# Kernel tuning notes

Hardware: AMD Instinct MI355X
Metric: run time of the kernel (lower is better)

## Reference

```python
import jax, jax.numpy as jnp
import numpy as np
import math

B = 2048
NOSC = 64            # oscillators per modality
M = 3                # modalities (audio, text, vision) in sorted order
BDIM = 256           # binding_dim
DT = 0.01
NSTEPS = 10
DIMS = [512, 768, 1024]  # audio, text, vision
TWO_PI = 2.0 * math.pi


def setup_inputs() -> dict:
    key = jax.random.key(0)
    ks = iter(jax.random.split(key, 40))
    d = {}
    names = ['a', 't', 'v']
    for name, dim, x_key in zip(names, DIMS, ['x_audio', 'x_text', 'x_vision']):
        d[x_key] = jax.random.normal(next(ks), (B, dim), dtype=jnp.float32)
        s = 1.0 / math.sqrt(dim)
        d[f'Wf_{name}'] = jax.random.uniform(next(ks), (BDIM, dim), jnp.float32, -s, s)
        d[f'bf_{name}'] = jax.random.uniform(next(ks), (BDIM,), jnp.float32, -s, s)
        d[f'Wp_{name}'] = jax.random.uniform(next(ks), (NOSC, dim), jnp.float32, -s, s)
        d[f'bp_{name}'] = jax.random.uniform(next(ks), (NOSC,), jnp.float32, -s, s)
    # omegas: randn*0.1 + 1.0 + i*0.5 for i-th sorted modality
    for i, name in enumerate(names):
        d[f'omega_{name}'] = jax.random.normal(next(ks), (NOSC,), jnp.float32) * 0.1 + 1.0 + i * 0.5
    N = M * NOSC
    d['inter_coupling'] = jax.random.normal(next(ks), (N, N), jnp.float32) * 0.1
    s = 1.0 / math.sqrt(BDIM * M)
    d['W_fusion'] = jax.random.uniform(next(ks), (BDIM, BDIM * M), jnp.float32, -s, s)
    d['b_fusion'] = jax.random.uniform(next(ks), (BDIM,), jnp.float32, -s, s)
    return d


def reference(x_audio, x_text, x_vision,
              Wf_a, bf_a, Wp_a, bp_a,
              Wf_t, bf_t, Wp_t, bp_t,
              Wf_v, bf_v, Wp_v, bp_v,
              omega_a, omega_t, omega_v,
              inter_coupling, W_fusion, b_fusion):
    def enc(x, Wf, bf, Wp, bp):
        encoded = x @ Wf.T + bf                       # (B, BDIM)
        phases = (x @ Wp.T + bp) % TWO_PI             # (B, NOSC)
        return encoded, phases

    e_a, p_a = enc(x_audio, Wf_a, bf_a, Wp_a, bp_a)
    e_t, p_t = enc(x_text, Wf_t, bf_t, Wp_t, bp_t)
    e_v, p_v = enc(x_vision, Wf_v, bf_v, Wp_v, bp_v)

    phases = jnp.concatenate([p_a, p_t, p_v], axis=-1)        # (B, N)
    omega = jnp.concatenate([omega_a, omega_t, omega_v])      # (N,)
    K = (inter_coupling + inter_coupling.T) * 0.5             # (N, N)
    N = phases.shape[-1]

    def step(ph, _):
        diff = ph[:, :, None] - ph[:, None, :]                # (B, N, N)
        forces = jnp.einsum('ij,bij->bi', K, jnp.sin(diff)) / N
        ph = (ph + DT * (omega[None, :] + forces)) % TWO_PI
        return ph, None

    phases, _ = jax.lax.scan(step, phases, None, length=NSTEPS)

    pm = [phases[:, i * NOSC:(i + 1) * NOSC] for i in range(M)]  # per-modality

    # PLV between banks a,b: |mean_{i,j} exp(i(a_i - b_j))| = R_a * R_b where
    # R = |mean_k exp(i phi_k)| (resultant length), computed with real math.
    R = jnp.stack([jnp.sqrt(jnp.mean(jnp.cos(p), -1) ** 2 +
                            jnp.mean(jnp.sin(p), -1) ** 2) for p in pm])  # (M, B)
    bm = jnp.mean(R[:, None, :] * R[None, :, :], axis=-1)      # (M, M)
    binding_matrix = jnp.where(jnp.eye(M, dtype=bool), 1.0, bm)

    fused_parts = []
    for e, p in zip([e_a, e_t, e_v], pm):
        phase_mod = jnp.mean(jnp.cos(p), axis=-1, keepdims=True)  # (B, 1)
        fused_parts.append(e * (0.5 + 0.5 * phase_mod))
    fused = jnp.concatenate(fused_parts, axis=-1)              # (B, M*BDIM)
    bound = fused @ W_fusion.T + b_fusion                      # (B, BDIM)

    triu = jnp.triu(jnp.ones((M, M), dtype=bool), k=1)
    total = jnp.sum(jnp.where(triu, binding_matrix, 0.0)) / triu.sum()
    total_binding = jnp.full((bound.shape[0],), total)

    return bound, binding_matrix, phases, total_binding
```

## Files before the change

### kernel.cpp

```cpp
#include <hip/hip_runtime.h>
#include <math.h>

typedef short bf16x8 __attribute__((ext_vector_type(8)));
typedef short bf16x4 __attribute__((ext_vector_type(4)));
typedef float f32x4  __attribute__((ext_vector_type(4)));

#define INV_2PI  0.15915494309189535f
#define TWO_PI_F 6.283185307179586f
#define FSCALE   8.2893199e-06f

static __device__ inline short f2bf(float f) {
    union { float f; unsigned u; } v; v.f = f;
    unsigned r = (v.u + 0x7FFFu + ((v.u >> 16) & 1u)) >> 16;
    return (short)r;
}
static __device__ inline float bf2f(short h) {
    union { unsigned u; float f; } v; v.u = ((unsigned)(unsigned short)h) << 16;
    return v.f;
}

__global__ __launch_bounds__(256) void front_kernel(
    const float* __restrict__ xa, const float* __restrict__ xt, const float* __restrict__ xv,
    const float* __restrict__ Wpa, const float* __restrict__ Wpt, const float* __restrict__ Wpv,
    const float* __restrict__ Wfa, const float* __restrict__ Wft, const float* __restrict__ Wfv,
    const float* __restrict__ Wfu,
    const float* __restrict__ IC,
    const float* __restrict__ oa, const float* __restrict__ ot, const float* __restrict__ ov,
    const float* __restrict__ bpa, const float* __restrict__ bpt, const float* __restrict__ bpv,
    float* __restrict__ partial, short* __restrict__ XB, short* __restrict__ WB,
    short* __restrict__ Kp,
    float* __restrict__ om_eff, float* __restrict__ bp_all, float* __restrict__ bacc)
{
    __shared__ alignas(16) float As[16][72];
    __shared__ alignas(16) float Bs[16][72];
    int b = blockIdx.x;
    int t = threadIdx.x;

    if (b < 576) {
        int slot = b % 18, rb = b / 18;
        int z = slot < 4 ? 0 : (slot < 10 ? 1 : 2);
        int chunk = slot - (z == 0 ? 0 : (z == 1 ? 4 : 10));
        const float* A = z == 0 ? xa : (z == 1 ? xt : xv);
        const float* W = z == 0 ? Wpa : (z == 1 ? Wpt : Wpv);
        short* XBz = XB + (z == 0 ? 0 : (z == 1 ? 1048576 : 2621440));
        int K = z == 0 ? 512 : (z == 1 ? 768 : 1024);
        int kb = chunk * 128;
        int m0 = rb * 64;

        int tx = t & 15, ty = t >> 4;
        int row = t >> 2, c4 = t & 3;

        float acc[4][4] = {};
        float4 ar = *(const float4*)&A[(size_t)(m0 + row) * K + kb + c4 * 4];
        float4 br = *(const float4*)&W[(size_t)row * K + kb + c4 * 4];

        for (int k0 = 0; k0 < 128; k0 += 16) {
            if (k0) __syncthreads();
            As[c4 * 4 + 0][row] = ar.x;
            As[c4 * 4 + 1][row] = ar.y;
            As[c4 * 4 + 2][row] = ar.z;
            As[c4 * 4 + 3][row] = ar.w;
            Bs[c4 * 4 + 0][row] = br.x;
            Bs[c4 * 4 + 1][row] = br.y;
            Bs[c4 * 4 + 2][row] = br.z;
            Bs[c4 * 4 + 3][row] = br.w;
            {
                bf16x4 h; h[0] = f2bf(ar.x); h[1] = f2bf(ar.y);
                h[2] = f2bf(ar.z); h[3] = f2bf(ar.w);
                *(bf16x4*)&XBz[(size_t)(m0 + row) * K + kb + k0 + c4 * 4] = h;
            }
            __syncthreads();
            if (k0 + 16 < 128) {
                ar = *(const float4*)&A[(size_t)(m0 + row) * K + kb + k0 + 16 + c4 * 4];
                br = *(const float4*)&W[(size_t)row * K + kb + k0 + 16 + c4 * 4];
            }
#pragma unroll
            for (int kk = 0; kk < 16; ++kk) {
                float4 aq = *(const float4*)&As[kk][ty * 4];
                float4 bq = *(const float4*)&Bs[kk][tx * 4];
                float av[4] = {aq.x, aq.y, aq.z, aq.w};
                float bv[4] = {bq.x, bq.y, bq.z, bq.w};
#pragma unroll
                for (int i = 0; i < 4; ++i)
#pragma unroll
                    for (int j = 0; j < 4; ++j)
                        acc[i][j] += av[i] * bv[j];
            }
        }

        float* P = partial + (size_t)slot * 131072;
#pragma unroll
        for (int i = 0; i < 4; ++i) {
            float4 v = make_float4(acc[i][0], acc[i][1], acc[i][2], acc[i][3]);
            *(float4*)&P[(size_t)(m0 + ty * 4 + i) * 64 + tx * 4] = v;
        }
    } else if (b < 600) {
        for (int u = (b - 576) * 256 + t; u < 196608; u += 24 * 256) {
            const float4* sp;
            if (u < 32768)       sp = (const float4*)Wfa + u;
            else if (u < 81920)  sp = (const float4*)Wft + (u - 32768);
            else if (u < 147456) sp = (const float4*)Wfv + (u - 81920);
            else                 sp = (const float4*)Wfu + (u - 147456);
            float4 v = *sp;
            bf16x4 h; h[0] = f2bf(v.x); h[1] = f2bf(v.y); h[2] = f2bf(v.z); h[3] = f2bf(v.w);
            *(bf16x4*)(WB + (size_t)u * 4) = h;
        }
    } else if (b < 632) {
        for (int idx = (b - 600) * 256 + t; idx < 36864; idx += 32 * 256) {
            int k = idx / 192, n = idx - k * 192;
            float v = 0.5f * (IC[k * 192 + n] + IC[n * 192 + k]);
            int nt = n >> 4, kc = k >> 5;
            int lane = ((k >> 3) & 3) * 16 + (n & 15);
            int j = k & 7;
            Kp[((nt * 6 + kc) * 64 + lane) * 8 + j] = f2bf(v);
        }
    } else {
        if (t < 192) {
            float w = t < 64 ? oa[t] : (t < 128 ? ot[t - 64] : ov[t - 128]);
            om_eff[t] = w * (0.01f * INV_2PI);
            float bb = t < 64 ? bpa[t] : (t < 128 ? bpt[t - 64] : bpv[t - 128]);
            bp_all[t] = bb;
        }
        if (t < 4) bacc[t] = 0.f;
    }
}

__global__ __launch_bounds__(256) void mid_kernel(
    const short* __restrict__ XB, const short* __restrict__ WB,
    const float* __restrict__ ba, const float* __restrict__ bt, const float* __restrict__ bv,
    const float* __restrict__ partial, const float* __restrict__ bp_all,
    const short* __restrict__ Kp, const float* __restrict__ om_eff,
    short* __restrict__ e_bf16,
    float* __restrict__ phases_out, float* __restrict__ pm, float* __restrict__ bacc)
{
    __shared__ alignas(16) char smem[26816];
    int b = blockIdx.x;
    int t = threadIdx.x;
    int lane = t & 63, w = t >> 6;
    int q = lane >> 4, col = lane & 15;

    if (b < 384) {
        int z = b / 128, r = b % 128;
        int m0 = (r >> 2) * 64, n0 = (r & 3) * 64;
        const short* A    = XB + (z == 0 ? 0 : (z == 1 ? 1048576 : 2621440));
        const short* W    = WB + (z == 0 ? 0 : (z == 1 ? 131072 : 327680));
        const float* bias = z == 0 ? ba : (z == 1 ? bt : bv);
        int K             = z == 0 ? 512 : (z == 1 ? 768 : 1024);

        short* As = (short*)smem;
        short* Bs = (short*)smem + 64 * 72;

        int srow = t >> 3, sc8 = t & 7;

        f32x4 acc[4];
#pragma unroll
        for (int f = 0; f < 4; ++f)
#pragma unroll
            for (int rr = 0; rr < 4; ++rr) acc[f][rr] = 0.f;

        bf16x8 av[2], bv8[2];
#pragma unroll
        for (int p = 0; p < 2; ++p) {
            av[p]  = *(const bf16x8*)&A[(size_t)(m0 + srow + 32 * p) * K + sc8 * 8];
            bv8[p] = *(const bf16x8*)&W[(size_t)(n0 + srow + 32 * p) * K + sc8 * 8];
        }

        for (int kb = 0; kb < K; kb += 64) {
            if (kb) __syncthreads();
#pragma unroll
            for (int p = 0; p < 2; ++p) {
                *(bf16x8*)&As[(srow + 32 * p) * 72 + sc8 * 8] = av[p];
                *(bf16x8*)&Bs[(srow + 32 * p) * 72 + sc8 * 8] = bv8[p];
            }
            __syncthreads();
            if (kb + 64 < K) {
#pragma unroll
                for (int p = 0; p < 2; ++p) {
                    av[p]  = *(const bf16x8*)&A[(size_t)(m0 + srow + 32 * p) * K + kb + 64 + sc8 * 8];
                    bv8[p] = *(const bf16x8*)&W[(size_t)(n0 + srow + 32 * p) * K + kb + 64 + sc8 * 8];
                }
            }

            bf16x8 bfr[2];
#pragma unroll
            for (int kc = 0; kc < 2; ++kc)
                bfr[kc] = *(const bf16x8*)&Bs[(w * 16 + col) * 72 + kc * 32 + q * 8];
#pragma unroll
            for (int f = 0; f < 4; ++f)
#pragma unroll
                for (int kc = 0; kc < 2; ++kc) {
                    bf16x8 af = *(const bf16x8*)&As[(f * 16 + col) * 72 + kc * 32 + q * 8];
                    acc[f] = __builtin_amdgcn_mfma_f32_16x16x32_bf16(af, bfr[kc], acc[f], 0, 0, 0);
                }
        }

        int n = n0 + w * 16 + col;
        float bn = bias[n];
#pragma unroll
        for (int f = 0; f < 4; ++f)
#pragma unroll
            for (int rr = 0; rr < 4; ++rr) {
                int m = m0 + f * 16 + q * 4 + rr;
                e_bf16[(size_t)m * 768 + z * 256 + n] = f2bf(acc[f][rr] + bn);
            }
    } else {
        short (*cs)[2][16][208] = (short (*)[2][16][208])smem;
        float (*Rl)[3] = (float (*)[3])(smem + 26624);

        int m0 = (b - 384) * 16;

        bf16x8 kb[3][6];
#pragma unroll
        for (int ntl = 0; ntl < 3; ++ntl)
#pragma unroll
            for (int kc = 0; kc < 6; ++kc) {
                int nt = w * 3 + ntl;
                kb[ntl][kc] = *(const bf16x8*)&Kp[((nt * 6 + kc) * 64 + lane) * 8];
            }

        float ph[3][4], om[3], c[3][4], s[3][4];
#pragma unroll
        for (int ntl = 0; ntl < 3; ++ntl) {
            int i = (w * 3 + ntl) * 16 + col;
            int z = i >> 6;
            int c0 = (z == 0) ? 0 : (z == 1 ? 4 : 10);
            int nch = (z == 0) ? 4 : (z == 1 ? 6 : 8);
            om[ntl] = om_eff[i];
#pragma unroll
            for (int r = 0; r < 4; ++r) {
                float raw = bp_all[i];
                size_t base = (size_t)c0 * 131072 + (size_t)(m0 + q * 4 + r) * 64 + (i & 63);
#pragma unroll
                for (int cc = 0; cc < 8; ++cc)
                    if (cc < nch) raw += partial[base + (size_t)cc * 131072];
                raw *= INV_2PI;
                ph[ntl][r] = raw - floorf(raw);
            }
        }

        for (int step = 0; step < 10; ++step) {
            int p = step & 1;
#pragma unroll
            for (int ntl = 0; ntl < 3; ++ntl) {
                int i = (w * 3 + ntl) * 16 + col;
#pragma unroll
                for (int r = 0; r < 4; ++r) {
                    c[ntl][r] = __builtin_amdgcn_cosf(ph[ntl][r]);
                    s[ntl][r] = __builtin_amdgcn_sinf(ph[ntl][r]);
                    cs[p][0][q * 4 + r][i] = f2bf(c[ntl][r]);
                    cs[p][1][q * 4 + r][i] = f2bf(s[ntl][r]);
                }
            }
            __syncthreads();

            f32x4 aC[3], aS[3];
#pragma unroll
            for (int ntl = 0; ntl < 3; ++ntl)
#pragma unroll
                for (int r = 0; r < 4; ++r) { aC[ntl][r] = 0.f; aS[ntl][r] = 0.f; }

#pragma unroll
            for (int kc = 0; kc < 6; ++kc) {
                bf16x8 ac  = *(const bf16x8*)&cs[p][0][col][kc * 32 + q * 8];
                bf16x8 as_ = *(const bf16x8*)&cs[p][1][col][kc * 32 + q * 8];
#pragma unroll
                for (int ntl = 0; ntl < 3; ++ntl) {
                    aC[ntl] = __builtin_amdgcn_mfma_f32_16x16x32_bf16(ac,  kb[ntl][kc], aC[ntl], 0, 0, 0);
                    aS[ntl] = __builtin_amdgcn_mfma_f32_16x16x32_bf16(as_, kb[ntl][kc], aS[ntl], 0, 0, 0);
                }
            }

#pragma unroll
            for (int ntl = 0; ntl < 3; ++ntl)
#pragma unroll
                for (int r = 0; r < 4; ++r) {
                    float f = (s[ntl][r] * aC[ntl][r] - c[ntl][r] * aS[ntl][r]) * FSCALE;
                    float pn = ph[ntl][r] + om[ntl] + f;
                    ph[ntl][r] = pn - floorf(pn);
                }
            if (step < 9) __syncthreads();
        }

        __syncthreads();
#pragma unroll
        for (int ntl = 0; ntl < 3; ++ntl) {
            int i = (w * 3 + ntl) * 16 + col;
#pragma unroll
            for (int r = 0; r < 4; ++r) {
                float cp = __builtin_amdgcn_cosf(ph[ntl][r]);
                float sp = __builtin_amdgcn_sinf(ph[ntl][r]);
                cs[0][0][q * 4 + r][i] = f2bf(cp);
                cs[0][1][q * 4 + r][i] = f2bf(sp);
                phases_out[(size_t)(m0 + q * 4 + r) * 192 + i] = ph[ntl][r] * TWO_PI_F;
            }
        }
        __syncthreads();

        if (t < 48) {
            int r = t & 15, mod = t >> 4;
            float sc = 0.f, ss = 0.f;
#pragma unroll
            for (int g = 0; g < 8; ++g) {
                bf16x8 vc = *(const bf16x8*)&cs[0][0][r][mod * 64 + g * 8];
                bf16x8 vs = *(const bf16x8*)&cs[0][1][r][mod * 64 + g * 8];
#pragma unroll
                for (int j = 0; j < 8; ++j) { sc += bf2f(vc[j]); ss += bf2f(vs[j]); }
            }
            sc *= (1.f / 64.f); ss *= (1.f / 64.f);
            pm[(size_t)(m0 + r) * 3 + mod] = 0.5f + 0.5f * sc;
            Rl[r][mod] = sqrtf(sc * sc + ss * ss);
        }
        __syncthreads();
        if (t < 3) {
            int a = (t == 2) ? 1 : 0;
            int bb = (t == 0) ? 1 : 2;
            float accp = 0.f;
            for (int r = 0; r < 16; ++r) accp += Rl[r][a] * Rl[r][bb];
            atomicAdd(&bacc[t], accp);
        }
    }
}

__global__ __launch_bounds__(256) void back_kernel(
    const short* __restrict__ e_bf16, const short* __restrict__ WB,
    const float* __restrict__ bias, const float* __restrict__ pm,
    const float* __restrict__ bacc,
    float* __restrict__ out_bound, float* __restrict__ out_bm, float* __restrict__ out_total)
{
    const short* Wfb = WB + 589824;
    int m0 = blockIdx.x * 32, n0 = blockIdx.y * 64;
    int t = threadIdx.x;
    int lane = t & 63, w = t >> 6;
    int q = lane >> 4, col = lane & 15;

    __shared__ alignas(16) short As[32 * 72];
    __shared__ alignas(16) short Bs[64 * 72];

    int srow = t >> 3, sc8 = t & 7;

    f32x4 acc[2];
#pragma unroll
    for (int f = 0; f < 2; ++f)
#pragma unroll
        for (int r = 0; r < 4; ++r) acc[f][r] = 0.f;

    bf16x8 av = *(const bf16x8*)&e_bf16[(size_t)(m0 + srow) * 768 + sc8 * 8];
    float asc = pm[(size_t)(m0 + srow) * 3 + 0];
    bf16x8 bv8[2];
#pragma unroll
    for (int p = 0; p < 2; ++p)
        bv8[p] = *(const bf16x8*)&Wfb[(size_t)(n0 + srow + 32 * p) * 768 + sc8 * 8];

    for (int kb = 0; kb < 768; kb += 64) {
        if (kb) __syncthreads();
        {
            bf16x8 h;
#pragma unroll
            for (int j = 0; j < 8; ++j) h[j] = f2bf(bf2f(av[j]) * asc);
            *(bf16x8*)&As[srow * 72 + sc8 * 8] = h;
        }
#pragma unroll
        for (int p = 0; p < 2; ++p)
            *(bf16x8*)&Bs[(srow + 32 * p) * 72 + sc8 * 8] = bv8[p];
        __syncthreads();
        if (kb + 64 < 768) {
            int k = kb + 64;
            av = *(const bf16x8*)&e_bf16[(size_t)(m0 + srow) * 768 + k + sc8 * 8];
            asc = pm[(size_t)(m0 + srow) * 3 + (k >> 8)];
#pragma unroll
            for (int p = 0; p < 2; ++p)
                bv8[p] = *(const bf16x8*)&Wfb[(size_t)(n0 + srow + 32 * p) * 768 + k + sc8 * 8];
        }

        bf16x8 bfr[2];
#pragma unroll
        for (int kc = 0; kc < 2; ++kc)
            bfr[kc] = *(const bf16x8*)&Bs[(w * 16 + col) * 72 + kc * 32 + q * 8];
#pragma unroll
        for (int f = 0; f < 2; ++f)
#pragma unroll
            for (int kc = 0; kc < 2; ++kc) {
                bf16x8 af = *(const bf16x8*)&As[(f * 16 + col) * 72 + kc * 32 + q * 8];
                acc[f] = __builtin_amdgcn_mfma_f32_16x16x32_bf16(af, bfr[kc], acc[f], 0, 0, 0);
            }
    }

    int n = n0 + w * 16 + col;
    float bn = bias[n];
#pragma unroll
    for (int f = 0; f < 2; ++f)
#pragma unroll
        for (int r = 0; r < 4; ++r) {
            int m = m0 + f * 16 + q * 4 + r;
            out_bound[(size_t)m * 256 + n] = acc[f][r] + bn;
        }

    if (blockIdx.x == 0 && blockIdx.y == 0) {
        float p01 = bacc[0] * (1.f / 2048.f);
        float p02 = bacc[1] * (1.f / 2048.f);
        float p12 = bacc[2] * (1.f / 2048.f);
        float total = (p01 + p02 + p12) * (1.f / 3.f);
        if (t == 0) {
            out_bm[0] = 1.f; out_bm[1] = p01; out_bm[2] = p02;
            out_bm[3] = p01; out_bm[4] = 1.f; out_bm[5] = p12;
            out_bm[6] = p02; out_bm[7] = p12; out_bm[8] = 1.f;
        }
        for (int i = t; i < 2048; i += 256) out_total[i] = total;
    }
}

extern "C" void kernel_launch(void* const* d_in, const int* in_sizes, int n_in,
                              void* d_out, int out_size, void* d_ws, size_t ws_size,
                              hipStream_t stream)
{
    const float* x_a  = (const float*)d_in[0];
    const float* Wf_a = (const float*)d_in[1];
    const float* bf_a = (const float*)d_in[2];
    const float* Wp_a = (const float*)d_in[3];
    const float* bp_a = (const float*)d_in[4];
    const float* x_t  = (const float*)d_in[5];
    const float* Wf_t = (const float*)d_in[6];
    const float* bf_t = (const float*)d_in[7];
    const float* Wp_t = (const float*)d_in[8];
    const float* bp_t = (const float*)d_in[9];
    const float* x_v  = (const float*)d_in[10];
    const float* Wf_v = (const float*)d_in[11];
    const float* bf_v = (const float*)d_in[12];
    const float* Wp_v = (const float*)d_in[13];
    const float* bp_v = (const float*)d_in[14];
    const float* om_a = (const float*)d_in[15];
    const float* om_t = (const float*)d_in[16];
    const float* om_v = (const float*)d_in[17];
    const float* IC   = (const float*)d_in[18];
    const float* Wfu  = (const float*)d_in[19];
    const float* bfu  = (const float*)d_in[20];

    float* ws      = (float*)d_ws;
    float* omw     = ws;
    float* bpw     = ws + 256;
    float* pmv     = ws + 512;
    float* baccw   = ws + 6656;
    float* partial = ws + 6720;
    short* e_bf    = (short*)(ws + 2366016);
    short* XB      = (short*)(ws + 3152448);
    short* Kpck    = (short*)(ws + 5511744);
    short* WB      = (short*)(ws + 5530176);

    float* out        = (float*)d_out;
    float* out_bound  = out;
    float* out_bm     = out + 524288;
    float* out_phases = out + 524297;
    float* out_total  = out + 917513;

    front_kernel<<<633, 256, 0, stream>>>(
        x_a, x_t, x_v, Wp_a, Wp_t, Wp_v, Wf_a, Wf_t, Wf_v, Wfu,
        IC, om_a, om_t, om_v, bp_a, bp_t, bp_v,
        partial, XB, WB, Kpck, omw, bpw, baccw);

    mid_kernel<<<512, 256, 0, stream>>>(
        XB, WB, bf_a, bf_t, bf_v,
        partial, bpw, Kpck, omw,
        e_bf, out_phases, pmv, baccw);

    dim3 gF(64, 4);
    back_kernel<<<gF, 256, 0, stream>>>(e_bf, WB, bfu, pmv, baccw,
                                        out_bound, out_bm, out_total);
}
```

Before: 157.4 us.

## Fuse encoder GEMM into front kernel and fusion GEMM into oscillator kernel

Moves the feature-encoder GEMM into the front kernel, which now converts fp32 inputs to bf16 on the fly instead of writing a bf16 copy of x and reading it back. The fusion GEMM and the binding finalisation move into the oscillator kernel, which takes over from the separate back kernel. A last-block atomic counter does the final write, so one launch and the phase-modulation buffer round trip go away. The trade-off is that the fused fusion GEMM now runs on only 128 blocks, and each block reads the whole fusion weight straight from global memory, so parallelism drops in that stage.

```diff
diff --git a/kernel.cpp b/kernel.cpp
--- a/kernel.cpp
+++ b/kernel.cpp
@@ -18,31 +18,37 @@
     union { unsigned u; float f; } v; v.u = ((unsigned)(unsigned short)h) << 16;
     return v.f;
 }
+static __device__ inline bf16x8 cvt8(float4 u, float4 v) {
+    bf16x8 h;
+    h[0] = f2bf(u.x); h[1] = f2bf(u.y); h[2] = f2bf(u.z); h[3] = f2bf(u.w);
+    h[4] = f2bf(v.x); h[5] = f2bf(v.y); h[6] = f2bf(v.z); h[7] = f2bf(v.w);
+    return h;
+}
 
 __global__ __launch_bounds__(256) void front_kernel(
     const float* __restrict__ xa, const float* __restrict__ xt, const float* __restrict__ xv,
     const float* __restrict__ Wpa, const float* __restrict__ Wpt, const float* __restrict__ Wpv,
     const float* __restrict__ Wfa, const float* __restrict__ Wft, const float* __restrict__ Wfv,
-    const float* __restrict__ Wfu,
-    const float* __restrict__ IC,
+    const float* __restrict__ bfa, const float* __restrict__ bft, const float* __restrict__ bfv,
+    const float* __restrict__ Wfu, const float* __restrict__ IC,
     const float* __restrict__ oa, const float* __restrict__ ot, const float* __restrict__ ov,
     const float* __restrict__ bpa, const float* __restrict__ bpt, const float* __restrict__ bpv,
-    float* __restrict__ partial, short* __restrict__ XB, short* __restrict__ WB,
+    float* __restrict__ partial, short* __restrict__ e_bf16, short* __restrict__ WB,
     short* __restrict__ Kp,
     float* __restrict__ om_eff, float* __restrict__ bp_all, float* __restrict__ bacc)
 {
-    __shared__ alignas(16) float As[16][72];
-    __shared__ alignas(16) float Bs[16][72];
+    __shared__ alignas(16) char smem[18432];
     int b = blockIdx.x;
     int t = threadIdx.x;
 
     if (b < 576) {
+        float (*As)[72] = (float (*)[72])smem;
+        float (*Bs)[72] = (float (*)[72])(smem + 4608);
         int slot = b % 18, rb = b / 18;
         int z = slot < 4 ? 0 : (slot < 10 ? 1 : 2);
         int chunk = slot - (z == 0 ? 0 : (z == 1 ? 4 : 10));
         const float* A = z == 0 ? xa : (z == 1 ? xt : xv);
         const float* W = z == 0 ? Wpa : (z == 1 ? Wpt : Wpv);
-        short* XBz = XB + (z == 0 ? 0 : (z == 1 ? 1048576 : 2621440));
         int K = z == 0 ? 512 : (z == 1 ? 768 : 1024);
         int kb = chunk * 128;
         int m0 = rb * 64;
@@ -64,11 +70,6 @@
             Bs[c4 * 4 + 1][row] = br.y;
             Bs[c4 * 4 + 2][row] = br.z;
             Bs[c4 * 4 + 3][row] = br.w;
-            {
-                bf16x4 h; h[0] = f2bf(ar.x); h[1] = f2bf(ar.y);
-                h[2] = f2bf(ar.z); h[3] = f2bf(ar.w);
-                *(bf16x4*)&XBz[(size_t)(m0 + row) * K + kb + k0 + c4 * 4] = h;
-            }
             __syncthreads();
             if (k0 + 16 < 128) {
                 ar = *(const float4*)&A[(size_t)(m0 + row) * K + kb + k0 + 16 + c4 * 4];
@@ -94,19 +95,89 @@
             float4 v = make_float4(acc[i][0], acc[i][1], acc[i][2], acc[i][3]);
             *(float4*)&P[(size_t)(m0 + ty * 4 + i) * 64 + tx * 4] = v;
         }
-    } else if (b < 600) {
-        for (int u = (b - 576) * 256 + t; u < 196608; u += 24 * 256) {
-            const float4* sp;
-            if (u < 32768)       sp = (const float4*)Wfa + u;
-            else if (u < 81920)  sp = (const float4*)Wft + (u - 32768);
-            else if (u < 147456) sp = (const float4*)Wfv + (u - 81920);
-            else                 sp = (const float4*)Wfu + (u - 147456);
-            float4 v = *sp;
+    } else if (b < 960) {
+        int bb = b - 576;
+        int z = bb >> 7, r = bb & 127;
+        int m0 = (r >> 2) * 64, n0 = (r & 3) * 64;
+        const float* A    = z == 0 ? xa : (z == 1 ? xt : xv);
+        const float* Wf   = z == 0 ? Wfa : (z == 1 ? Wft : Wfv);
+        const float* bias = z == 0 ? bfa : (z == 1 ? bft : bfv);
+        int K             = z == 0 ? 512 : (z == 1 ? 768 : 1024);
+
+        short* As = (short*)smem;
+        short* Bs = (short*)smem + 64 * 72;
+
+        int lane = t & 63, w = t >> 6;
+        int q = lane >> 4, col = lane & 15;
+        int srow = t >> 3, sc8 = t & 7;
+
+        f32x4 acc[4];
+#pragma unroll
+        for (int f = 0; f < 4; ++f)
+#pragma unroll
+            for (int rr = 0; rr < 4; ++rr) acc[f][rr] = 0.f;
+
+        float4 a0[2], a1[2], b0[2], b1[2];
+#pragma unroll
+        for (int p = 0; p < 2; ++p) {
+            int rw = srow + 32 * p;
+            a0[p] = *(const float4*)&A[(size_t)(m0 + rw) * K + sc8 * 8];
+            a1[p] = *(const float4*)&A[(size_t)(m0 + rw) * K + sc8 * 8 + 4];
+            b0[p] = *(const float4*)&Wf[(size_t)(n0 + rw) * K + sc8 * 8];
+            b1[p] = *(const float4*)&Wf[(size_t)(n0 + rw) * K + sc8 * 8 + 4];
+        }
+
+        for (int kb = 0; kb < K; kb += 64) {
+            if (kb) __syncthreads();
+#pragma unroll
+            for (int p = 0; p < 2; ++p) {
+                int rw = srow + 32 * p;
+                *(bf16x8*)&As[rw * 72 + sc8 * 8] = cvt8(a0[p], a1[p]);
+                *(bf16x8*)&Bs[rw * 72 + sc8 * 8] = cvt8(b0[p], b1[p]);
+            }
+            __syncthreads();
+            if (kb + 64 < K) {
+                int k = kb + 64;
+#pragma unroll
+                for (int p = 0; p < 2; ++p) {
+                    int rw = srow + 32 * p;
+                    a0[p] = *(const float4*)&A[(size_t)(m0 + rw) * K + k + sc8 * 8];
+                    a1[p] = *(const float4*)&A[(size_t)(m0 + rw) * K + k + sc8 * 8 + 4];
+                    b0[p] = *(const float4*)&Wf[(size_t)(n0 + rw) * K + k + sc8 * 8];
+                    b1[p] = *(const float4*)&Wf[(size_t)(n0 + rw) * K + k + sc8 * 8 + 4];
+                }
+            }
+
+            bf16x8 bfr[2];
+#pragma unroll
+            for (int kc = 0; kc < 2; ++kc)
+                bfr[kc] = *(const bf16x8*)&Bs[(w * 16 + col) * 72 + kc * 32 + q * 8];
+#pragma unroll
+            for (int f = 0; f < 4; ++f)
+#pragma unroll
+                for (int kc = 0; kc < 2; ++kc) {
+                    bf16x8 af = *(const bf16x8*)&As[(f * 16 + col) * 72 + kc * 32 + q * 8];
+                    acc[f] = __builtin_amdgcn_mfma_f32_16x16x32_bf16(af, bfr[kc], acc[f], 0, 0, 0);
+                }
+        }
+
+        int n = n0 + w * 16 + col;
+        float bn = bias[n];
+#pragma unroll
+        for (int f = 0; f < 4; ++f)
+#pragma unroll
+            for (int rr = 0; rr < 4; ++rr) {
+                int m = m0 + f * 16 + q * 4 + rr;
+                e_bf16[(size_t)m * 768 + z * 256 + n] = f2bf(acc[f][rr] + bn);
+            }
+    } else if (b < 972) {
+        for (int u = (b - 960) * 256 + t; u < 49152; u += 12 * 256) {
+            float4 v = ((const float4*)Wfu)[u];
             bf16x4 h; h[0] = f2bf(v.x); h[1] = f2bf(v.y); h[2] = f2bf(v.z); h[3] = f2bf(v.w);
             *(bf16x4*)(WB + (size_t)u * 4) = h;
         }
-    } else if (b < 632) {
-        for (int idx = (b - 600) * 256 + t; idx < 36864; idx += 32 * 256) {
+    } else if (b < 1004) {
+        for (int idx = (b - 972) * 256 + t; idx < 36864; idx += 32 * 256) {
             int k = idx / 192, n = idx - k * 192;
             float v = 0.5f * (IC[k * 192 + n] + IC[n * 192 + k]);
             int nt = n >> 4, kc = k >> 5;
@@ -121,290 +192,200 @@
             float bb = t < 64 ? bpa[t] : (t < 128 ? bpt[t - 64] : bpv[t - 128]);
             bp_all[t] = bb;
         }
-        if (t < 4) bacc[t] = 0.f;
+        if (t < 8) bacc[t] = 0.f;
     }
 }
 
 __global__ __launch_bounds__(256) void mid_kernel(
-    const short* __restrict__ XB, const short* __restrict__ WB,
-    const float* __restrict__ ba, const float* __restrict__ bt, const float* __restrict__ bv,
     const float* __restrict__ partial, const float* __restrict__ bp_all,
     const short* __restrict__ Kp, const float* __restrict__ om_eff,
-    short* __restrict__ e_bf16,
-    float* __restrict__ phases_out, float* __restrict__ pm, float* __restrict__ bacc)
+    const short* __restrict__ e_bf16, const short* __restrict__ WB,
+    const float* __restrict__ bfu,
+    float* __restrict__ phases_out, float* __restrict__ bacc,
+    float* __restrict__ out_bound, float* __restrict__ out_bm, float* __restrict__ out_total)
 {
-    __shared__ alignas(16) char smem[26816];
+    __shared__ alignas(16) char smem[27040];
+    short (*cs)[2][16][208] = (short (*)[2][16][208])smem;
+    float (*Rl)[3]  = (float (*)[3])(smem + 26624);
+    float (*scl)[3] = (float (*)[3])(smem + 26816);
+    float* fin      = (float*)(smem + 27008);
+    unsigned* dflag = (unsigned*)(smem + 27024);
+
     int b = blockIdx.x;
     int t = threadIdx.x;
     int lane = t & 63, w = t >> 6;
     int q = lane >> 4, col = lane & 15;
-
-    if (b < 384) {
-        int z = b / 128, r = b % 128;
-        int m0 = (r >> 2) * 64, n0 = (r & 3) * 64;
-        const short* A    = XB + (z == 0 ? 0 : (z == 1 ? 1048576 : 2621440));
-        const short* W    = WB + (z == 0 ? 0 : (z == 1 ? 131072 : 327680));
-        const float* bias = z == 0 ? ba : (z == 1 ? bt : bv);
-        int K             = z == 0 ? 512 : (z == 1 ? 768 : 1024);
-
-        short* As = (short*)smem;
-        short* Bs = (short*)smem + 64 * 72;
-
-        int srow = t >> 3, sc8 = t & 7;
-
-        f32x4 acc[4];
-#pragma unroll
-        for (int f = 0; f < 4; ++f)
-#pragma unroll
-            for (int rr = 0; rr < 4; ++rr) acc[f][rr] = 0.f;
-
-        bf16x8 av[2], bv8[2];
-#pragma unroll
-        for (int p = 0; p < 2; ++p) {
-            av[p]  = *(const bf16x8*)&A[(size_t)(m0 + srow + 32 * p) * K + sc8 * 8];
-            bv8[p] = *(const bf16x8*)&W[(size_t)(n0 + srow + 32 * p) * K + sc8 * 8];
-        }
-
-        for (int kb = 0; kb < K; kb += 64) {
-            if (kb) __syncthreads();
-#pragma unroll
-            for (int p = 0; p < 2; ++p) {
-                *(bf16x8*)&As[(srow + 32 * p) * 72 + sc8 * 8] = av[p];
-                *(bf16x8*)&Bs[(srow + 32 * p) * 72 + sc8 * 8] = bv8[p];
-            }
-            __syncthreads();
-            if (kb + 64 < K) {
-#pragma unroll
-                for (int p = 0; p < 2; ++p) {
-                    av[p]  = *(const bf16x8*)&A[(size_t)(m0 + srow + 32 * p) * K + kb + 64 + sc8 * 8];
-                    bv8[p] = *(const bf16x8*)&W[(size_t)(n0 + srow + 32 * p) * K + kb + 64 + sc8 * 8];
-                }
-            }
-
-            bf16x8 bfr[2];
-#pragma unroll
-            for (int kc = 0; kc < 2; ++kc)
-                bfr[kc] = *(const bf16x8*)&Bs[(w * 16 + col) * 72 + kc * 32 + q * 8];
-#pragma unroll
-            for (int f = 0; f < 4; ++f)
-#pragma unroll
-                for (int kc = 0; kc < 2; ++kc) {
-                    bf16x8 af = *(const bf16x8*)&As[(f * 16 + col) * 72 + kc * 32 + q * 8];
-                    acc[f] = __builtin_amdgcn_mfma_f32_16x16x32_bf16(af, bfr[kc], acc[f], 0, 0, 0);
-                }
-        }
-
-        int n = n0 + w * 16 + col;
-        float bn = bias[n];
-#pragma unroll
-        for (int f = 0; f < 4; ++f)
-#pragma unroll
-            for (int rr = 0; rr < 4; ++rr) {
-                int m = m0 + f * 16 + q * 4 + rr;
-                e_bf16[(size_t)m * 768 + z * 256 + n] = f2bf(acc[f][rr] + bn);
-            }
-    } else {
-        short (*cs)[2][16][208] = (short (*)[2][16][208])smem;
-        float (*Rl)[3] = (float (*)[3])(smem + 26624);
-
-        int m0 = (b - 384) * 16;
-
-        bf16x8 kb[3][6];
-#pragma unroll
-        for (int ntl = 0; ntl < 3; ++ntl)
-#pragma unroll
-            for (int kc = 0; kc < 6; ++kc) {
-                int nt = w * 3 + ntl;
-                kb[ntl][kc] = *(const bf16x8*)&Kp[((nt * 6 + kc) * 64 + lane) * 8];
-            }
-
-        float ph[3][4], om[3], c[3][4], s[3][4];
+    int m0 = b * 16;
+
+    bf16x8 kb_[3][6];
+#pragma unroll
+    for (int ntl = 0; ntl < 3; ++ntl)
+#pragma unroll
+        for (int kc = 0; kc < 6; ++kc) {
+            int nt = w * 3 + ntl;
+            kb_[ntl][kc] = *(const bf16x8*)&Kp[((nt * 6 + kc) * 64 + lane) * 8];
+        }
+
+    float ph[3][4], om[3], c[3][4], s[3][4];
+#pragma unroll
+    for (int ntl = 0; ntl < 3; ++ntl) {
+        int i = (w * 3 + ntl) * 16 + col;
+        int z = i >> 6;
+        int c0 = (z == 0) ? 0 : (z == 1 ? 4 : 10);
+        int nch = (z == 0) ? 4 : (z == 1 ? 6 : 8);
+        om[ntl] = om_eff[i];
+#pragma unroll
+        for (int r = 0; r < 4; ++r) {
+            float raw = bp_all[i];
+            size_t base = (size_t)c0 * 131072 + (size_t)(m0 + q * 4 + r) * 64 + (i & 63);
+#pragma unroll
+            for (int cc = 0; cc < 8; ++cc)
+                if (cc < nch) raw += partial[base + (size_t)cc * 131072];
+            raw *= INV_2PI;
+            ph[ntl][r] = raw - floorf(raw);
+        }
+    }
+
+    for (int step = 0; step < 10; ++step) {
+        int p = step & 1;
 #pragma unroll
         for (int ntl = 0; ntl < 3; ++ntl) {
             int i = (w * 3 + ntl) * 16 + col;
-            int z = i >> 6;
-            int c0 = (z == 0) ? 0 : (z == 1 ? 4 : 10);
-            int nch = (z == 0) ? 4 : (z == 1 ? 6 : 8);
-            om[ntl] = om_eff[i];
 #pragma unroll
             for (int r = 0; r < 4; ++r) {
-                float raw = bp_all[i];
-                size_t base = (size_t)c0 * 131072 + (size_t)(m0 + q * 4 + r) * 64 + (i & 63);
-#pragma unroll
-                for (int cc = 0; cc < 8; ++cc)
-                    if (cc < nch) raw += partial[base + (size_t)cc * 131072];
-                raw *= INV_2PI;
-                ph[ntl][r] = raw - floorf(raw);
-            }
-        }
-
-        for (int step = 0; step < 10; ++step) {
-            int p = step & 1;
+                c[ntl][r] = __builtin_amdgcn_cosf(ph[ntl][r]);
+                s[ntl][r] = __builtin_amdgcn_sinf(ph[ntl][r]);
+                cs[p][0][q * 4 + r][i] = f2bf(c[ntl][r]);
+                cs[p][1][q * 4 + r][i] = f2bf(s[ntl][r]);
+            }
+        }
+        __syncthreads();
+
+        f32x4 aC[3], aS[3];
+#pragma unroll
+        for (int ntl = 0; ntl < 3; ++ntl)
+#pragma unroll
+            for (int r = 0; r < 4; ++r) { aC[ntl][r] = 0.f; aS[ntl][r] = 0.f; }
+
+#pragma unroll
+        for (int kc = 0; kc < 6; ++kc) {
+            bf16x8 ac  = *(const bf16x8*)&cs[p][0][col][kc * 32 + q * 8];
+            bf16x8 as_ = *(const bf16x8*)&cs[p][1][col][kc * 32 + q * 8];
 #pragma unroll
             for (int ntl = 0; ntl < 3; ++ntl) {
-                int i = (w * 3 + ntl) * 16 + col;
-#pragma unroll
-                for (int r = 0; r < 4; ++r) {
-                    c[ntl][r] = __builtin_amdgcn_cosf(ph[ntl][r]);
-                    s[ntl][r] = __builtin_amdgcn_sinf(ph[ntl][r]);
-                    cs[p][0][q * 4 + r][i] = f2bf(c[ntl][r]);
-                    cs[p][1][q * 4 + r][i] = f2bf(s[ntl][r]);
-                }
-            }
-            __syncthreads();
-
-            f32x4 aC[3], aS[3];
-#pragma unroll
-            for (int ntl = 0; ntl < 3; ++ntl)
-#pragma unroll
-                for (int r = 0; r < 4; ++r) { aC[ntl][r] = 0.f; aS[ntl][r] = 0.f; }
-
-#pragma unroll
-            for (int kc = 0; kc < 6; ++kc) {
-                bf16x8 ac  = *(const bf16x8*)&cs[p][0][col][kc * 32 + q * 8];
-                bf16x8 as_ = *(const bf16x8*)&cs[p][1][col][kc * 32 + q * 8];
-#pragma unroll
-                for (int ntl = 0; ntl < 3; ++ntl) {
-                    aC[ntl] = __builtin_amdgcn_mfma_f32_16x16x32_bf16(ac,  kb[ntl][kc], aC[ntl], 0, 0, 0);
-                    aS[ntl] = __builtin_amdgcn_mfma_f32_16x16x32_bf16(as_, kb[ntl][kc], aS[ntl], 0, 0, 0);
-                }
-            }
-
-#pragma unroll
-            for (int ntl = 0; ntl < 3; ++ntl)
-#pragma unroll
-                for (int r = 0; r < 4; ++r) {
-                    float f = (s[ntl][r] * aC[ntl][r] - c[ntl][r] * aS[ntl][r]) * FSCALE;
-                    float pn = ph[ntl][r] + om[ntl] + f;
-                    ph[ntl][r] = pn - floorf(pn);
-                }
-            if (step < 9) __syncthreads();
-        }
-
-        __syncthreads();
-#pragma unroll
-        for (int ntl = 0; ntl < 3; ++ntl) {
-            int i = (w * 3 + ntl) * 16 + col;
+                aC[ntl] = __builtin_amdgcn_mfma_f32_16x16x32_bf16(ac,  kb_[ntl][kc], aC[ntl], 0, 0, 0);
+                aS[ntl] = __builtin_amdgcn_mfma_f32_16x16x32_bf16(as_, kb_[ntl][kc], aS[ntl], 0, 0, 0);
+            }
+        }
+
+#pragma unroll
+        for (int ntl = 0; ntl < 3; ++ntl)
 #pragma unroll
             for (int r = 0; r < 4; ++r) {
-                float cp = __builtin_amdgcn_cosf(ph[ntl][r]);
-                float sp = __builtin_amdgcn_sinf(ph[ntl][r]);
-                cs[0][0][q * 4 + r][i] = f2bf(cp);
-                cs[0][1][q * 4 + r][i] = f2bf(sp);
-                phases_out[(size_t)(m0 + q * 4 + r) * 192 + i] = ph[ntl][r] * TWO_PI_F;
-            }
-        }
-        __syncthreads();
-
-        if (t < 48) {
-            int r = t & 15, mod = t >> 4;
-            float sc = 0.f, ss = 0.f;
-#pragma unroll
-            for (int g = 0; g < 8; ++g) {
-                bf16x8 vc = *(const bf16x8*)&cs[0][0][r][mod * 64 + g * 8];
-                bf16x8 vs = *(const bf16x8*)&cs[0][1][r][mod * 64 + g * 8];
-#pragma unroll
-                for (int j = 0; j < 8; ++j) { sc += bf2f(vc[j]); ss += bf2f(vs[j]); }
-            }
-            sc *= (1.f / 64.f); ss *= (1.f / 64.f);
-            pm[(size_t)(m0 + r) * 3 + mod] = 0.5f + 0.5f * sc;
-            Rl[r][mod] = sqrtf(sc * sc + ss * ss);
-        }
-        __syncthreads();
-        if (t < 3) {
-            int a = (t == 2) ? 1 : 0;
-            int bb = (t == 0) ? 1 : 2;
-            float accp = 0.f;
-            for (int r = 0; r < 16; ++r) accp += Rl[r][a] * Rl[r][bb];
-            atomicAdd(&bacc[t], accp);
-        }
-    }
-}
-
-__global__ __launch_bounds__(256) void back_kernel(
-    const short* __restrict__ e_bf16, const short* __restrict__ WB,
-    const float* __restrict__ bias, const float* __restrict__ pm,
-    const float* __restrict__ bacc,
-    float* __restrict__ out_bound, float* __restrict__ out_bm, float* __restrict__ out_total)
-{
-    const short* Wfb = WB + 589824;
-    int m0 = blockIdx.x * 32, n0 = blockIdx.y * 64;
-    int t = threadIdx.x;
-    int lane = t & 63, w = t >> 6;
-    int q = lane >> 4, col = lane & 15;
-
-    __shared__ alignas(16) short As[32 * 72];
-    __shared__ alignas(16) short Bs[64 * 72];
-
-    int srow = t >> 3, sc8 = t & 7;
-
-    f32x4 acc[2];
-#pragma unroll
-    for (int f = 0; f < 2; ++f)
-#pragma unroll
-        for (int r = 0; r < 4; ++r) acc[f][r] = 0.f;
-
-    bf16x8 av = *(const bf16x8*)&e_bf16[(size_t)(m0 + srow) * 768 + sc8 * 8];
-    float asc = pm[(size_t)(m0 + srow) * 3 + 0];
-    bf16x8 bv8[2];
-#pragma unroll
-    for (int p = 0; p < 2; ++p)
-        bv8[p] = *(const bf16x8*)&Wfb[(size_t)(n0 + srow + 32 * p) * 768 + sc8 * 8];
-
-    for (int kb = 0; kb < 768; kb += 64) {
-        if (kb) __syncthreads();
-        {
-            bf16x8 h;
-#pragma unroll
-            for (int j = 0; j < 8; ++j) h[j] = f2bf(bf2f(av[j]) * asc);
-            *(bf16x8*)&As[srow * 72 + sc8 * 8] = h;
-        }
-#pragma unroll
-        for (int p = 0; p < 2; ++p)
-            *(bf16x8*)&Bs[(srow + 32 * p) * 72 + sc8 * 8] = bv8[p];
-        __syncthreads();
-        if (kb + 64 < 768) {
-            int k = kb + 64;
-            av = *(const bf16x8*)&e_bf16[(size_t)(m0 + srow) * 768 + k + sc8 * 8];
-            asc = pm[(size_t)(m0 + srow) * 3 + (k >> 8)];
-#pragma unroll
-            for (int p = 0; p < 2; ++p)
-                bv8[p] = *(const bf16x8*)&Wfb[(size_t)(n0 + srow + 32 * p) * 768 + k + sc8 * 8];
-        }
-
-        bf16x8 bfr[2];
-#pragma unroll
-        for (int kc = 0; kc < 2; ++kc)
-            bfr[kc] = *(const bf16x8*)&Bs[(w * 16 + col) * 72 + kc * 32 + q * 8];
-#pragma unroll
-        for (int f = 0; f < 2; ++f)
-#pragma unroll
-            for (int kc = 0; kc < 2; ++kc) {
-                bf16x8 af = *(const bf16x8*)&As[(f * 16 + col) * 72 + kc * 32 + q * 8];
-                acc[f] = __builtin_amdgcn_mfma_f32_16x16x32_bf16(af, bfr[kc], acc[f], 0, 0, 0);
-            }
-    }
-
-    int n = n0 + w * 16 + col;
-    float bn = bias[n];
-#pragma unroll
-    for (int f = 0; f < 2; ++f)
+                float f = (s[ntl][r] * aC[ntl][r] - c[ntl][r] * aS[ntl][r]) * FSCALE;
+                float pn = ph[ntl][r] + om[ntl] + f;
+                ph[ntl][r] = pn - floorf(pn);
+            }
+        if (step < 9) __syncthreads();
+    }
+
+    __syncthreads();
+#pragma unroll
+    for (int ntl = 0; ntl < 3; ++ntl) {
+        int i = (w * 3 + ntl) * 16 + col;
 #pragma unroll
         for (int r = 0; r < 4; ++r) {
-            int m = m0 + f * 16 + q * 4 + r;
-            out_bound[(size_t)m * 256 + n] = acc[f][r] + bn;
-        }
-
-    if (blockIdx.x == 0 && blockIdx.y == 0) {
-        float p01 = bacc[0] * (1.f / 2048.f);
-        float p02 = bacc[1] * (1.f / 2048.f);
-        float p12 = bacc[2] * (1.f / 2048.f);
-        float total = (p01 + p02 + p12) * (1.f / 3.f);
+            float cp = __builtin_amdgcn_cosf(ph[ntl][r]);
+            float sp = __builtin_amdgcn_sinf(ph[ntl][r]);
+            cs[0][0][q * 4 + r][i] = f2bf(cp);
+            cs[0][1][q * 4 + r][i] = f2bf(sp);
+            phases_out[(size_t)(m0 + q * 4 + r) * 192 + i] = ph[ntl][r] * TWO_PI_F;
+        }
+    }
+    __syncthreads();
+
+    if (t < 48) {
+        int r = t & 15, mod = t >> 4;
+        float sc = 0.f, ss = 0.f;
+#pragma unroll
+        for (int g = 0; g < 8; ++g) {
+            bf16x8 vc = *(const bf16x8*)&cs[0][0][r][mod * 64 + g * 8];
+            bf16x8 vs = *(const bf16x8*)&cs[0][1][r][mod * 64 + g * 8];
+#pragma unroll
+            for (int j = 0; j < 8; ++j) { sc += bf2f(vc[j]); ss += bf2f(vs[j]); }
+        }
+        sc *= (1.f / 64.f); ss *= (1.f / 64.f);
+        scl[r][mod] = 0.5f + 0.5f * sc;
+        Rl[r][mod]  = sqrtf(sc * sc + ss * ss);
+    }
+    __syncthreads();
+
+    if (t < 3) {
+        int a = (t == 2) ? 1 : 0;
+        int bb2 = (t == 0) ? 1 : 2;
+        float accp = 0.f;
+        for (int r = 0; r < 16; ++r) accp += Rl[r][a] * Rl[r][bb2];
+        atomicAdd(&bacc[t], accp);
+    }
+
+    short* As2 = (short*)smem;
+#pragma unroll
+    for (int i = 0; i < 6; ++i) {
+        int g = t + 256 * i;
+        int rw = g / 96, cg = g - rw * 96;
+        float sc = scl[rw][cg >> 5];
+        bf16x8 v = *(const bf16x8*)&e_bf16[(size_t)(m0 + rw) * 768 + cg * 8];
+        bf16x8 h;
+#pragma unroll
+        for (int j = 0; j < 8; ++j) h[j] = f2bf(bf2f(v[j]) * sc);
+        *(bf16x8*)&As2[rw * 776 + cg * 8] = h;
+    }
+    __syncthreads();
+
+    f32x4 facc[4];
+#pragma unroll
+    for (int j = 0; j < 4; ++j)
+#pragma unroll
+        for (int rr = 0; rr < 4; ++rr) facc[j][rr] = 0.f;
+
+    for (int k0 = 0; k0 < 768; k0 += 32) {
+        bf16x8 af = *(const bf16x8*)&As2[col * 776 + k0 + q * 8];
+#pragma unroll
+        for (int j = 0; j < 4; ++j) {
+            int n = (w * 4 + j) * 16 + col;
+            bf16x8 bfr = *(const bf16x8*)&WB[(size_t)n * 768 + k0 + q * 8];
+            facc[j] = __builtin_amdgcn_mfma_f32_16x16x32_bf16(af, bfr, facc[j], 0, 0, 0);
+        }
+    }
+
+#pragma unroll
+    for (int j = 0; j < 4; ++j) {
+        int n = (w * 4 + j) * 16 + col;
+        float bn = bfu[n];
+#pragma unroll
+        for (int rr = 0; rr < 4; ++rr) {
+            int m = m0 + q * 4 + rr;
+            out_bound[(size_t)m * 256 + n] = facc[j][rr] + bn;
+        }
+    }
+
+    __threadfence();
+    __syncthreads();
+    if (t == 0)
+        *dflag = (atomicAdd((unsigned*)(bacc + 4), 1u) == 127u) ? 1u : 0u;
+    __syncthreads();
+    if (*dflag) {
         if (t == 0) {
+            float p01 = atomicAdd(&bacc[0], 0.f) * (1.f / 2048.f);
+            float p02 = atomicAdd(&bacc[1], 0.f) * (1.f / 2048.f);
+            float p12 = atomicAdd(&bacc[2], 0.f) * (1.f / 2048.f);
             out_bm[0] = 1.f; out_bm[1] = p01; out_bm[2] = p02;
             out_bm[3] = p01; out_bm[4] = 1.f; out_bm[5] = p12;
             out_bm[6] = p02; out_bm[7] = p12; out_bm[8] = 1.f;
-        }
+            fin[0] = (p01 + p02 + p12) * (1.f / 3.f);
+        }
+        __syncthreads();
+        float total = fin[0];
         for (int i = t; i < 2048; i += 256) out_total[i] = total;
     }
 }
@@ -438,13 +419,11 @@
     float* ws      = (float*)d_ws;
     float* omw     = ws;
     float* bpw     = ws + 256;
-    float* pmv     = ws + 512;
-    float* baccw   = ws + 6656;
-    float* partial = ws + 6720;
-    short* e_bf    = (short*)(ws + 2366016);
-    short* XB      = (short*)(ws + 3152448);
-    short* Kpck    = (short*)(ws + 5511744);
-    short* WB      = (short*)(ws + 5530176);
+    float* baccw   = ws + 512;
+    float* partial = ws + 576;
+    short* e_bf    = (short*)(ws + 2359872);
+    short* Kpck    = (short*)(ws + 3146304);
+    short* WB      = (short*)(ws + 3164736);
 
     float* out        = (float*)d_out;
     float* out_bound  = out;
@@ -452,17 +431,12 @@
     float* out_phases = out + 524297;
     float* out_total  = out + 917513;
 
-    front_kernel<<<633, 256, 0, stream>>>(
-        x_a, x_t, x_v, Wp_a, Wp_t, Wp_v, Wf_a, Wf_t, Wf_v, Wfu,
-        IC, om_a, om_t, om_v, bp_a, bp_t, bp_v,
-        partial, XB, WB, Kpck, omw, bpw, baccw);
-
-    mid_kernel<<<512, 256, 0, stream>>>(
-        XB, WB, bf_a, bf_t, bf_v,
-        partial, bpw, Kpck, omw,
-        e_bf, out_phases, pmv, baccw);
-
-    dim3 gF(64, 4);
-    back_kernel<<<gF, 256, 0, stream>>>(e_bf, WB, bfu, pmv, baccw,
-                                        out_bound, out_bm, out_total);
-}
+    front_kernel<<<1005, 256, 0, stream>>>(
+        x_a, x_t, x_v, Wp_a, Wp_t, Wp_v, Wf_a, Wf_t, Wf_v,
+        bf_a, bf_t, bf_v, Wfu, IC, om_a, om_t, om_v, bp_a, bp_t, bp_v,
+        partial, e_bf, WB, Kpck, omw, bpw, baccw);
+
+    mid_kernel<<<128, 256, 0, stream>>>(
+        partial, bpw, Kpck, omw, e_bf, WB, bfu,
+        out_phases, baccw, out_bound, out_bm, out_total);
+}
```

After: 178.8 us. 1.14x slower.

## Drop redundant barriers in oscillator loop and restage fusion GEMM with full-K LDS tile

Applied to the files above, without the earlier changes.

In the phase-integration branch of mid_kernel, the cos/sin staging rows are padded from 208 to 216 shorts. The per-step barrier and the post-loop barrier are removed, relying on the existing double-buffered cs[p] layout. back_kernel is restructured: each block loads its whole scaled 16x768 activation tile into LDS once, then streams W_fusion fragments straight from global memory into registers with one-step prefetch. This avoids the per-K-chunk LDS staging and barriers, and the grid changes to 128x2 blocks of 16 rows by 128 columns. Removing the barriers could race if a warp overwrites cs while another warp is still reading it.

```diff
diff --git a/kernel.cpp b/kernel.cpp
--- a/kernel.cpp
+++ b/kernel.cpp
@@ -133,7 +133,7 @@
     short* __restrict__ e_bf16,
     float* __restrict__ phases_out, float* __restrict__ pm, float* __restrict__ bacc)
 {
-    __shared__ alignas(16) char smem[26816];
+    __shared__ alignas(16) char smem[27840];
     int b = blockIdx.x;
     int t = threadIdx.x;
     int lane = t & 63, w = t >> 6;
@@ -204,8 +204,8 @@
                 e_bf16[(size_t)m * 768 + z * 256 + n] = f2bf(acc[f][rr] + bn);
             }
     } else {
-        short (*cs)[2][16][208] = (short (*)[2][16][208])smem;
-        float (*Rl)[3] = (float (*)[3])(smem + 26624);
+        short (*cs)[2][16][216] = (short (*)[2][16][216])smem;
+        float (*Rl)[3] = (float (*)[3])(smem + 27648);
 
         int m0 = (b - 384) * 16;
 
@@ -278,10 +278,8 @@
                     float pn = ph[ntl][r] + om[ntl] + f;
                     ph[ntl][r] = pn - floorf(pn);
                 }
-            if (step < 9) __syncthreads();
-        }
-
-        __syncthreads();
+        }
+
 #pragma unroll
         for (int ntl = 0; ntl < 3; ++ntl) {
             int i = (w * 3 + ntl) * 16 + col;
@@ -328,72 +326,64 @@
     float* __restrict__ out_bound, float* __restrict__ out_bm, float* __restrict__ out_total)
 {
     const short* Wfb = WB + 589824;
-    int m0 = blockIdx.x * 32, n0 = blockIdx.y * 64;
+    __shared__ alignas(16) short As2[16 * 776];
+
+    int m0 = blockIdx.x * 16, n0 = blockIdx.y * 128;
     int t = threadIdx.x;
     int lane = t & 63, w = t >> 6;
     int q = lane >> 4, col = lane & 15;
 
-    __shared__ alignas(16) short As[32 * 72];
-    __shared__ alignas(16) short Bs[64 * 72];
-
-    int srow = t >> 3, sc8 = t & 7;
-
-    f32x4 acc[2];
-#pragma unroll
-    for (int f = 0; f < 2; ++f)
-#pragma unroll
-        for (int r = 0; r < 4; ++r) acc[f][r] = 0.f;
-
-    bf16x8 av = *(const bf16x8*)&e_bf16[(size_t)(m0 + srow) * 768 + sc8 * 8];
-    float asc = pm[(size_t)(m0 + srow) * 3 + 0];
-    bf16x8 bv8[2];
-#pragma unroll
-    for (int p = 0; p < 2; ++p)
-        bv8[p] = *(const bf16x8*)&Wfb[(size_t)(n0 + srow + 32 * p) * 768 + sc8 * 8];
-
-    for (int kb = 0; kb < 768; kb += 64) {
-        if (kb) __syncthreads();
-        {
-            bf16x8 h;
-#pragma unroll
-            for (int j = 0; j < 8; ++j) h[j] = f2bf(bf2f(av[j]) * asc);
-            *(bf16x8*)&As[srow * 72 + sc8 * 8] = h;
-        }
-#pragma unroll
-        for (int p = 0; p < 2; ++p)
-            *(bf16x8*)&Bs[(srow + 32 * p) * 72 + sc8 * 8] = bv8[p];
-        __syncthreads();
-        if (kb + 64 < 768) {
-            int k = kb + 64;
-            av = *(const bf16x8*)&e_bf16[(size_t)(m0 + srow) * 768 + k + sc8 * 8];
-            asc = pm[(size_t)(m0 + srow) * 3 + (k >> 8)];
-#pragma unroll
-            for (int p = 0; p < 2; ++p)
-                bv8[p] = *(const bf16x8*)&Wfb[(size_t)(n0 + srow + 32 * p) * 768 + k + sc8 * 8];
-        }
-
-        bf16x8 bfr[2];
-#pragma unroll
-        for (int kc = 0; kc < 2; ++kc)
-            bfr[kc] = *(const bf16x8*)&Bs[(w * 16 + col) * 72 + kc * 32 + q * 8];
-#pragma unroll
-        for (int f = 0; f < 2; ++f)
-#pragma unroll
-            for (int kc = 0; kc < 2; ++kc) {
-                bf16x8 af = *(const bf16x8*)&As[(f * 16 + col) * 72 + kc * 32 + q * 8];
-                acc[f] = __builtin_amdgcn_mfma_f32_16x16x32_bf16(af, bfr[kc], acc[f], 0, 0, 0);
-            }
-    }
-
-    int n = n0 + w * 16 + col;
-    float bn = bias[n];
-#pragma unroll
-    for (int f = 0; f < 2; ++f)
-#pragma unroll
-        for (int r = 0; r < 4; ++r) {
-            int m = m0 + f * 16 + q * 4 + r;
-            out_bound[(size_t)m * 256 + n] = acc[f][r] + bn;
-        }
+#pragma unroll
+    for (int i = 0; i < 6; ++i) {
+        int g = t + 256 * i;
+        int rw = g / 96, cg = g - rw * 96;
+        float sc = pm[(size_t)(m0 + rw) * 3 + (cg >> 5)];
+        bf16x8 v = *(const bf16x8*)&e_bf16[(size_t)(m0 + rw) * 768 + cg * 8];
+        bf16x8 h;
+#pragma unroll
+        for (int j = 0; j < 8; ++j) h[j] = f2bf(bf2f(v[j]) * sc);
+        *(bf16x8*)&As2[rw * 776 + cg * 8] = h;
+    }
+    __syncthreads();
+
+    f32x4 facc[2];
+#pragma unroll
+    for (int j = 0; j < 2; ++j)
+#pragma unroll
+        for (int rr = 0; rr < 4; ++rr) facc[j][rr] = 0.f;
+
+    int n_[2];
+#pragma unroll
+    for (int j = 0; j < 2; ++j) n_[j] = n0 + (w * 2 + j) * 16 + col;
+
+    bf16x8 bcur[2], bnxt[2];
+#pragma unroll
+    for (int j = 0; j < 2; ++j)
+        bcur[j] = *(const bf16x8*)&Wfb[(size_t)n_[j] * 768 + q * 8];
+
+    for (int k0 = 0; k0 < 768; k0 += 32) {
+        if (k0 + 32 < 768) {
+#pragma unroll
+            for (int j = 0; j < 2; ++j)
+                bnxt[j] = *(const bf16x8*)&Wfb[(size_t)n_[j] * 768 + k0 + 32 + q * 8];
+        }
+        bf16x8 af = *(const bf16x8*)&As2[col * 776 + k0 + q * 8];
+#pragma unroll
+        for (int j = 0; j < 2; ++j)
+            facc[j] = __builtin_amdgcn_mfma_f32_16x16x32_bf16(af, bcur[j], facc[j], 0, 0, 0);
+#pragma unroll
+        for (int j = 0; j < 2; ++j) bcur[j] = bnxt[j];
+    }
+
+#pragma unroll
+    for (int j = 0; j < 2; ++j) {
+        float bn = bias[n_[j]];
+#pragma unroll
+        for (int rr = 0; rr < 4; ++rr) {
+            int m = m0 + q * 4 + rr;
+            out_bound[(size_t)m * 256 + n_[j]] = facc[j][rr] + bn;
+        }
+    }
 
     if (blockIdx.x == 0 && blockIdx.y == 0) {
         float p01 = bacc[0] * (1.f / 2048.f);
@@ -462,7 +452,7 @@
         partial, bpw, Kpck, omw,
         e_bf, out_phases, pmv, baccw);
 
-    dim3 gF(64, 4);
+    dim3 gF(128, 2);
     back_kernel<<<gF, 256, 0, stream>>>(e_bf, WB, bfu, pmv, baccw,
                                         out_bound, out_bm, out_total);
 }
```

Measured after the change: 158.8 us. About the same (+0.8%).
